# Kernel tuning notes

Hardware: AMD Instinct MI355X
Metric: run time of the kernel (lower is better)

Reference implementation:

```python
import jax, jax.numpy as jnp
import numpy as np

IN_DIM, HID, HEADS, LAYERS = 15, 128, 8, 6
N_NODES, N_EDGES = 20000, 160000
HC = HEADS * HID  # 1024
LN_EPS = 1e-5


def setup_inputs() -> dict:
    key = jax.random.key(0)
    ks = jax.random.split(key, 12)
    w = lambda k, shape: (jax.random.normal(k, shape, jnp.float32) * 0.02)
    return {
        "x": jax.random.normal(ks[0], (N_NODES, IN_DIM), jnp.float32),
        "edge_index": jax.random.randint(ks[1], (2, N_EDGES), 0, N_NODES, jnp.int32),
        # input projection
        "Win": w(ks[2], (IN_DIM, HID)), "b_in": jnp.zeros((HID,), jnp.float32),
        # per-layer TransformerConv params (stacked over LAYERS)
        "Wq": w(ks[3], (LAYERS, HID, HC)), "bq": jnp.zeros((LAYERS, HC), jnp.float32),
        "Wk": w(ks[4], (LAYERS, HID, HC)), "bk": jnp.zeros((LAYERS, HC), jnp.float32),
        "Wv": w(ks[5], (LAYERS, HID, HC)), "bv": jnp.zeros((LAYERS, HC), jnp.float32),
        "Wskip": w(ks[6], (LAYERS, HID, HC)), "bskip": jnp.zeros((LAYERS, HC), jnp.float32),
        "Wbeta": w(ks[7], (LAYERS, 3 * HC, 1)),  # lin_beta, bias=False
        # LayerNorm(hid*heads) and output proj per layer
        "ln_g": jnp.ones((LAYERS, HC), jnp.float32), "ln_b": jnp.zeros((LAYERS, HC), jnp.float32),
        "Wproj": w(ks[8], (LAYERS, HC, HID)), "bproj": jnp.zeros((LAYERS, HID), jnp.float32),
    }


def _transformer_layer(h, src, dst, Wq, bq, Wk, bk, Wv, bv, Wskip, bskip, Wbeta, ln_g, ln_b, Wproj, bproj):
    N = h.shape[0]
    # multi-head q/k/v: [N, H, C]
    q = (h @ Wq + bq).reshape(N, HEADS, HID)
    k = (h @ Wk + bk).reshape(N, HEADS, HID)
    v = (h @ Wv + bv).reshape(N, HEADS, HID)
    # per-edge attention logits: [E, H]
    alpha = jnp.einsum("ehc,ehc->eh", q[dst], k[src]) / jnp.sqrt(jnp.float32(HID))
    # segment softmax over incoming edges of each destination node
    amax = jax.ops.segment_max(alpha, dst, num_segments=N)  # [N, H]
    ex = jnp.exp(alpha - amax[dst])
    denom = jax.ops.segment_sum(ex, dst, num_segments=N)  # [N, H]
    attn = ex / (denom[dst] + 1e-16)  # [E, H]
    # weighted message scatter-sum: [N, H, C] -> concat [N, H*C]
    msg = v[src] * attn[:, :, None]
    out = jax.ops.segment_sum(msg, dst, num_segments=N).reshape(N, HC)
    # beta-gated skip (beta=True, concat=True)
    x_r = h @ Wskip + bskip  # [N, HC]
    beta = jax.nn.sigmoid(jnp.concatenate([out, x_r, out - x_r], axis=-1) @ Wbeta)  # [N, 1]
    out = beta * x_r + (1.0 - beta) * out
    # LayerNorm over last dim (HC)
    mu = jnp.mean(out, axis=-1, keepdims=True)
    var = jnp.var(out, axis=-1, keepdims=True)
    out = (out - mu) * jax.lax.rsqrt(var + LN_EPS) * ln_g + ln_b
    # project back, residual, relu
    out = out @ Wproj + bproj
    return jax.nn.relu(out + h)


def reference(x, edge_index, Win, b_in, Wq, bq, Wk, bk, Wv, bv, Wskip, bskip, Wbeta, ln_g, ln_b, Wproj, bproj):
    src, dst = edge_index[0], edge_index[1]
    h = x @ Win + b_in  # input_lin; dropout is identity in eval
    for l in range(LAYERS):
        h = _transformer_layer(h, src, dst, Wq[l], bq[l], Wk[l], bk[l], Wv[l], bv[l],
                               Wskip[l], bskip[l], Wbeta[l], ln_g[l], ln_b[l], Wproj[l], bproj[l])
    return h
```

## Files before the change

### kernel.cpp

```cpp
#include <hip/hip_runtime.h>
#include <stdint.h>

#define NN 20000
#define NE 160000
#define L_IN 15
#define D_H 128
#define N_HEADS 8
#define D_HC 1024
#define N_LAYERS 6
#define M_PAD 20096
#define QS2 2048

typedef unsigned short u16;
typedef __attribute__((ext_vector_type(8))) short short8;
typedef __attribute__((ext_vector_type(4))) float f32x4;

#define RSQRT_D 0.08838834764831845f

__device__ __forceinline__ float bu2f(u16 u) { return __uint_as_float(((unsigned)u) << 16); }
__device__ __forceinline__ u16 f2bu(float f) {
    unsigned x = __float_as_uint(f);
    return (u16)((x + 0x7fffu + ((x >> 16) & 1u)) >> 16);
}
__device__ __forceinline__ float wred64(float v) {
#pragma unroll
    for (int m = 32; m >= 1; m >>= 1) v += __shfl_xor(v, m, 64);
    return v;
}
__device__ __forceinline__ void cvt16(const uint4& u0, const uint4& u1, float* f) {
    unsigned d[8] = {u0.x, u0.y, u0.z, u0.w, u1.x, u1.y, u1.z, u1.w};
#pragma unroll
    for (int i = 0; i < 8; i++) {
        f[2 * i]     = __uint_as_float(d[i] << 16);
        f[2 * i + 1] = __uint_as_float(d[i] & 0xffff0000u);
    }
}

__global__ void k_detect(const u16* __restrict__ xb, int* __restrict__ flag) {
    int t = threadIdx.x;
    u16 u = xb[2 * t];
    int e = (u >> 7) & 0xFF;
    int weird = (e > 150 || (e != 0 && e < 100)) ? 1 : 0;
    __shared__ int cnt;
    if (t == 0) cnt = 0;
    __syncthreads();
    atomicAdd(&cnt, weird);
    __syncthreads();
    if (t == 0) *flag = (cnt > 64) ? 1 : 0;
}

struct CvDesc { const void* in[13]; u16* out[13]; };
#define CV_TOTAL 1930976
__global__ void k_convert_all(CvDesc dsc, const int* __restrict__ flag) {
    const int sizes[13] = {NN * L_IN, L_IN * D_H, D_H,
                           N_LAYERS * D_HC, N_LAYERS * D_HC, N_LAYERS * D_HC,
                           N_LAYERS * D_HC, N_LAYERS * 3 * D_HC,
                           N_LAYERS * D_HC, N_LAYERS * D_HC, N_LAYERS * D_H,
                           N_LAYERS * D_H * D_HC, N_LAYERS * D_H * D_HC};
    int off = blockIdx.x * 256 + threadIdx.x;
    if (off >= CV_TOTAL) return;
    int seg = 0;
#pragma unroll
    for (int s = 0; s < 13; s++) {
        if (off >= sizes[s] && seg == s) { off -= sizes[s]; seg = s + 1; }
    }
    if (*flag) dsc.out[seg][off] = f2bu(((const float*)dsc.in[seg])[off]);
    else       dsc.out[seg][off] = ((const u16*)dsc.in[seg])[off];
}

__global__ void k_zero(int* __restrict__ p, int n) {
    int i = blockIdx.x * 256 + threadIdx.x;
    if (i < n) p[i] = 0;
}

__global__ void k_convT_vs(const void* __restrict__ Wv, const void* __restrict__ Ws,
                           u16* __restrict__ WvT, u16* __restrict__ Bmain,
                           const int* __restrict__ flag) {
    __shared__ u16 tile[64][66];
    int tk = blockIdx.x, tn = blockIdx.y, l = blockIdx.z;
    int t = threadIdx.x;
    int isv = (tn < 16);
    const void* W = isv ? Wv : Ws;
    int n_off = (tn & 15) * 64;
    int r = t >> 2, c0 = (t & 3) * 16;
    size_t base = (size_t)l * 128 * 1024 + (size_t)(tk * 64 + r) * 1024 + n_off + c0;
    if (*flag) {
        const float* Wf = (const float*)W;
#pragma unroll
        for (int cc = 0; cc < 16; cc++) tile[c0 + cc][r] = f2bu(Wf[base + cc]);
    } else {
        const u16* Wh = (const u16*)W;
#pragma unroll
        for (int cc = 0; cc < 16; cc++) tile[c0 + cc][r] = Wh[base + cc];
    }
    __syncthreads();
    int i = t >> 2, j0 = (t & 3) * 16;
    u16* dst = isv ? (WvT + ((size_t)l * 1024 + n_off + i) * 128 + tk * 64 + j0)
                   : (Bmain + ((size_t)l * 2048 + 1024 + n_off + i) * 128 + tk * 64 + j0);
#pragma unroll
    for (int jj = 0; jj < 16; jj++) dst[jj] = tile[i][j0 + jj];
}

__global__ void k_convT_proj(const void* __restrict__ Wp, u16* __restrict__ WT,
                             const int* __restrict__ flag) {
    __shared__ u16 tile[64][66];
    int tk = blockIdx.x, tn = blockIdx.y, l = blockIdx.z;
    int t = threadIdx.x;
    int r = t >> 2, c0 = (t & 3) * 16;
    size_t base = (size_t)l * 1024 * 128 + (size_t)(tk * 64 + r) * 128 + tn * 64 + c0;
    if (*flag) {
        const float* Wf = (const float*)Wp;
#pragma unroll
        for (int cc = 0; cc < 16; cc++) tile[c0 + cc][r] = f2bu(Wf[base + cc]);
    } else {
        const u16* Wh = (const u16*)Wp;
#pragma unroll
        for (int cc = 0; cc < 16; cc++) tile[c0 + cc][r] = Wh[base + cc];
    }
    __syncthreads();
    int i = t >> 2, j0 = (t & 3) * 16;
    u16* dst = WT + ((size_t)l * 128 + tn * 64 + i) * 1024 + tk * 64 + j0;
#pragma unroll
    for (int jj = 0; jj < 16; jj++) dst[jj] = tile[i][j0 + jj];
}

__global__ void k_GG(const u16* __restrict__ Wqb, const u16* __restrict__ Wkb,
                     u16* __restrict__ Bmain) {
    int h = blockIdx.x, l = blockIdx.y;
    __shared__ __align__(16) u16 Als[128 * 32];
    __shared__ __align__(16) u16 Bls[128 * 32];
    const int t = threadIdx.x;
    const int wave = t >> 6, lane = t & 63, quad = lane >> 4, l16 = lane & 15;
    const int wm = (wave >> 1) * 64, wn = (wave & 1) * 64;
    const u16* Ab = Wqb + (size_t)l * 128 * 1024 + h * 128;
    const u16* Bb = Wkb + (size_t)l * 128 * 1024 + h * 128;
    f32x4 acc[4][4];
#pragma unroll
    for (int i = 0; i < 4; i++)
#pragma unroll
        for (int j = 0; j < 4; j++) acc[i][j] = (f32x4){0.f, 0.f, 0.f, 0.f};
    for (int ko = 0; ko < 128; ko += 32) {
#pragma unroll
        for (int c = t; c < 512; c += 256) {
            int row = c >> 2, kc = c & 3;
            *reinterpret_cast<uint4*>(&Als[row * 32 + kc * 8]) =
                *reinterpret_cast<const uint4*>(Ab + (size_t)row * 1024 + ko + kc * 8);
            *reinterpret_cast<uint4*>(&Bls[row * 32 + kc * 8]) =
                *reinterpret_cast<const uint4*>(Bb + (size_t)row * 1024 + ko + kc * 8);
        }
        __syncthreads();
        short8 af[4], bf[4];
#pragma unroll
        for (int mt = 0; mt < 4; mt++)
            af[mt] = *reinterpret_cast<const short8*>(&Als[(wm + mt * 16 + l16) * 32 + quad * 8]);
#pragma unroll
        for (int nt = 0; nt < 4; nt++)
            bf[nt] = *reinterpret_cast<const short8*>(&Bls[(wn + nt * 16 + l16) * 32 + quad * 8]);
#pragma unroll
        for (int mt = 0; mt < 4; mt++)
#pragma unroll
            for (int nt = 0; nt < 4; nt++)
                acc[mt][nt] = __builtin_amdgcn_mfma_f32_16x16x32_bf16(af[mt], bf[nt], acc[mt][nt], 0, 0, 0);
        __syncthreads();
    }
    u16* dst = Bmain + (size_t)l * 2048 * 128;
#pragma unroll
    for (int mt = 0; mt < 4; mt++)
#pragma unroll
        for (int r = 0; r < 4; r++) {
            int row = wm + mt * 16 + quad * 4 + r;
#pragma unroll
            for (int nt = 0; nt < 4; nt++) {
                int col = wn + nt * 16 + l16;
                dst[(size_t)(h * 128 + col) * 128 + row] = f2bu(acc[mt][nt][r] * RSQRT_D);
            }
        }
}

__global__ void k_pre_small(const u16* __restrict__ Wqb, const u16* __restrict__ Wkb,
                            const u16* __restrict__ bq, const u16* __restrict__ bk,
                            u16* __restrict__ cb, float* __restrict__ wscT,
                            float* __restrict__ csc) {
    int gid = blockIdx.x * 256 + threadIdx.x;
    if (gid >= N_LAYERS * 2056) return;
    int l = gid / 2056, r = gid % 2056;
    float acc = 0.f;
    if (r < 1024) {
        int h = r >> 7, b = r & 127;
        const u16* bqp = bq + l * D_HC + h * 128;
        const u16* wkp = Wkb + (size_t)l * 128 * 1024 + (size_t)b * 1024 + h * 128;
        for (int m = 0; m < 128; m++) acc += bu2f(bqp[m]) * bu2f(wkp[m]);
        cb[l * 1024 + r] = f2bu(acc * RSQRT_D);
    } else if (r < 2048) {
        int idx = r - 1024;
        int h = idx >> 7, a = idx & 127;
        const u16* wqp = Wqb + (size_t)l * 128 * 1024 + (size_t)a * 1024 + h * 128;
        const u16* bkp = bk + l * D_HC + h * 128;
        for (int m = 0; m < 128; m++) acc += bu2f(wqp[m]) * bu2f(bkp[m]);
        wscT[l * 1024 + idx] = acc * RSQRT_D;
    } else {
        int h = r - 2048;
        const u16* bqp = bq + l * D_HC + h * 128;
        const u16* bkp = bk + l * D_HC + h * 128;
        for (int m = 0; m < 128; m++) acc += bu2f(bqp[m]) * bu2f(bkp[m]);
        csc[l * 8 + h] = acc * RSQRT_D;
    }
}

__global__ void k_input_proj(const u16* __restrict__ x, const u16* __restrict__ Win,
                             const u16* __restrict__ b_in, u16* __restrict__ h) {
    int gid = blockIdx.x * 256 + threadIdx.x;
    int n = gid >> 7, j = gid & 127;
    float acc = bu2f(b_in[j]);
#pragma unroll
    for (int i = 0; i < L_IN; i++) acc += bu2f(x[n * L_IN + i]) * bu2f(Win[i * D_H + j]);
    h[gid] = f2bu(acc);
}

__global__ void k_hist(const int* __restrict__ dst, int* __restrict__ cnt) {
    int e = blockIdx.x * 256 + threadIdx.x;
    if (e < NE) atomicAdd(&cnt[dst[e]], 1);
}
__global__ void k_scanA(const int* __restrict__ cnt, int* __restrict__ incl, int* __restrict__ bsum) {
    __shared__ int s[256];
    int b = blockIdx.x, t = threadIdx.x, i = b * 256 + t;
    int v = (i < NN) ? cnt[i] : 0;
    s[t] = v;
    __syncthreads();
    for (int off = 1; off < 256; off <<= 1) {
        int u = (t >= off) ? s[t - off] : 0;
        __syncthreads();
        s[t] += u;
        __syncthreads();
    }
    if (i < NN) incl[i] = s[t];
    if (t == 255) bsum[b] = s[255];
}
__global__ void k_scanB(const int* __restrict__ bsum, int* __restrict__ bpre, int nb) {
    __shared__ int s[128];
    int t = threadIdx.x;
    int v = (t < nb) ? bsum[t] : 0;
    s[t] = v;
    __syncthreads();
    for (int off = 1; off < 128; off <<= 1) {
        int u = (t >= off) ? s[t - off] : 0;
        __syncthreads();
        s[t] += u;
        __syncthreads();
    }
    if (t < nb) bpre[t] = s[t] - v;
}
__global__ void k_scanC(const int* __restrict__ incl, const int* __restrict__ bpre, int* __restrict__ offs) {
    int b = blockIdx.x, t = threadIdx.x, i = b * 256 + t;
    if (i < NN) offs[i + 1] = incl[i] + bpre[b];
    if (i == 0) offs[0] = 0;
}
__global__ void k_scatter(const int* __restrict__ dst, const int* __restrict__ src,
                          const int* __restrict__ offs, int* __restrict__ cursor,
                          int* __restrict__ srcp) {
    int e = blockIdx.x * 256 + threadIdx.x;
    if (e < NE) {
        int d = dst[e];
        int p = offs[d] + atomicAdd(&cursor[d], 1);
        srcp[p] = src[e];
    }
}

__global__ void k_gemm(const u16* __restrict__ A, int lda, int K,
                       const u16* __restrict__ Bt,
                       u16* __restrict__ C, int ldc,
                       const u16* __restrict__ bia0, const u16* __restrict__ bia1) {
    __shared__ __align__(16) u16 smem[128 * 136];
    u16* Als = smem;
    u16* Bls = smem + 4096;
    const int m0 = blockIdx.y * 128, n0 = blockIdx.x * 128;
    const int t = threadIdx.x;
    const int wave = t >> 6, lane = t & 63, quad = lane >> 4, l16 = lane & 15;
    const int wm = (wave >> 1) * 64, wn = (wave & 1) * 64;
    f32x4 acc[4][4];
#pragma unroll
    for (int i = 0; i < 4; i++)
#pragma unroll
        for (int j = 0; j < 4; j++) acc[i][j] = (f32x4){0.f, 0.f, 0.f, 0.f};

    for (int ko = 0; ko < K; ko += 32) {
#pragma unroll
        for (int c = t; c < 512; c += 256) {
            int row = c >> 2, kc = c & 3;
            *reinterpret_cast<uint4*>(&Als[row * 32 + kc * 8]) =
                *reinterpret_cast<const uint4*>(A + (size_t)(m0 + row) * lda + ko + kc * 8);
            *reinterpret_cast<uint4*>(&Bls[row * 32 + kc * 8]) =
                *reinterpret_cast<const uint4*>(Bt + (size_t)(n0 + row) * K + ko + kc * 8);
        }
        __syncthreads();
        short8 af[4], bf[4];
#pragma unroll
        for (int mt = 0; mt < 4; mt++)
            af[mt] = *reinterpret_cast<const short8*>(&Als[(wm + mt * 16 + l16) * 32 + quad * 8]);
#pragma unroll
        for (int nt = 0; nt < 4; nt++)
            bf[nt] = *reinterpret_cast<const short8*>(&Bls[(wn + nt * 16 + l16) * 32 + quad * 8]);
#pragma unroll
        for (int mt = 0; mt < 4; mt++)
#pragma unroll
            for (int nt = 0; nt < 4; nt++)
                acc[mt][nt] = __builtin_amdgcn_mfma_f32_16x16x32_bf16(af[mt], bf[nt], acc[mt][nt], 0, 0, 0);
        __syncthreads();
    }
#pragma unroll
    for (int mt = 0; mt < 4; mt++)
#pragma unroll
        for (int r = 0; r < 4; r++) {
            int rl = wm + mt * 16 + quad * 4 + r;
#pragma unroll
            for (int nt = 0; nt < 4; nt++) {
                int cl = wn + nt * 16 + l16;
                int col = n0 + cl;
                const u16* bp = (col < 1024) ? bia0 : bia1;
                smem[rl * 136 + cl] = f2bu(acc[mt][nt][r] + bu2f(bp[col & 1023]));
            }
        }
    __syncthreads();
#pragma unroll
    for (int c = t; c < 2048; c += 256) {
        int row = c >> 4, kc = c & 15;
        int grow = m0 + row;
        if (grow < NN)
            *reinterpret_cast<uint4*>(C + (size_t)grow * ldc + n0 + kc * 8) =
                *reinterpret_cast<const uint4*>(&smem[row * 136 + kc * 8]);
    }
}

__global__ void k_attn2(u16* __restrict__ qkvs2, const u16* __restrict__ hc,
                        const int* __restrict__ offs, const int* __restrict__ srcp,
                        const float* __restrict__ wscT_l, const float* __restrict__ csc_l) {
    int gid = blockIdx.x * 256 + threadIdx.x;
    int d = gid >> 6, lane = gid & 63;
    if (d >= NN) return;
    int hh = lane >> 3, ci = (lane & 7) * 16;
    u16* zp = qkvs2 + (size_t)d * QS2 + hh * 128 + ci;
    float zf[16];
    {
        uint4 z0 = *reinterpret_cast<const uint4*>(zp);
        uint4 z1 = *reinterpret_cast<const uint4*>(zp + 8);
        cvt16(z0, z1, zf);
    }
    float scown;
    {
        const u16* hdp = hc + (size_t)d * 128 + ci;
        uint4 hd0 = *reinterpret_cast<const uint4*>(hdp);
        uint4 hd1 = *reinterpret_cast<const uint4*>(hdp + 8);
        float hdf[16];
        cvt16(hd0, hd1, hdf);
        const float* wt = wscT_l + hh * 128 + ci;
        float scp = 0.f;
#pragma unroll
        for (int j = 0; j < 16; j++) scp += hdf[j] * wt[j];
        scp += __shfl_xor(scp, 1, 64);
        scp += __shfl_xor(scp, 2, 64);
        scp += __shfl_xor(scp, 4, 64);
        scown = scp + csc_l[hh];
    }
    float u[16];
#pragma unroll
    for (int j = 0; j < 16; j++) u[j] = 0.f;
    float lrun = 0.f;

    int beg = offs[d], end = offs[d + 1];
    for (int c0 = beg; c0 < end; c0 += 64) {
        int cn = min(64, end - c0);
        int myidx = (c0 + lane < end) ? srcp[c0 + lane] : 0;
        int s = __shfl(myidx, 0, 64);
        const u16* hp = hc + (size_t)s * 128 + ci;
        uint4 a0 = *reinterpret_cast<const uint4*>(hp);
        uint4 a1 = *reinterpret_cast<const uint4*>(hp + 8);
        for (int i = 0; i < cn; i++) {
            uint4 n0 = a0, n1 = a1;
            if (i + 1 < cn) {
                int sn = __shfl(myidx, i + 1, 64);
                const u16* hpn = hc + (size_t)sn * 128 + ci;
                n0 = *reinterpret_cast<const uint4*>(hpn);
                n1 = *reinterpret_cast<const uint4*>(hpn + 8);
            }
            float hf[16];
            cvt16(a0, a1, hf);
            float p = 0.f;
#pragma unroll
            for (int j = 0; j < 16; j++) p += zf[j] * hf[j];
            p += __shfl_xor(p, 1, 64);
            p += __shfl_xor(p, 2, 64);
            p += __shfl_xor(p, 4, 64);
            float w = __expf(p + scown);
            lrun += w;
#pragma unroll
            for (int j = 0; j < 16; j++) u[j] += w * hf[j];
            a0 = n0; a1 = n1;
        }
    }
    float inv = 1.f / (lrun + 1e-16f);
    unsigned out[8];
#pragma unroll
    for (int j = 0; j < 8; j++)
        out[j] = (unsigned)f2bu(u[2 * j] * inv) | ((unsigned)f2bu(u[2 * j + 1] * inv) << 16);
    uint4* op = reinterpret_cast<uint4*>(zp);
    op[0] = make_uint4(out[0], out[1], out[2], out[3]);
    op[1] = make_uint4(out[4], out[5], out[6], out[7]);
}

__global__ void k_vproj(const u16* __restrict__ A ,
                        const u16* __restrict__ WvT_l, const u16* __restrict__ bv_l,
                        u16* __restrict__ obuf) {
    __shared__ __align__(16) u16 smem[128 * 136];
    u16* Als = smem;
    u16* Bls = smem + 4096;
    const int m0 = blockIdx.x * 128, h = blockIdx.y;
    const int t = threadIdx.x;
    const int wave = t >> 6, lane = t & 63, quad = lane >> 4, l16 = lane & 15;
    const int wm = (wave >> 1) * 64, wn = (wave & 1) * 64;
    f32x4 acc[4][4];
#pragma unroll
    for (int i = 0; i < 4; i++)
#pragma unroll
        for (int j = 0; j < 4; j++) acc[i][j] = (f32x4){0.f, 0.f, 0.f, 0.f};

    for (int ko = 0; ko < 128; ko += 32) {
#pragma unroll
        for (int c = t; c < 512; c += 256) {
            int row = c >> 2, kc = c & 3;
            *reinterpret_cast<uint4*>(&Als[row * 32 + kc * 8]) =
                *reinterpret_cast<const uint4*>(A + (size_t)(m0 + row) * QS2 + h * 128 + ko + kc * 8);
            *reinterpret_cast<uint4*>(&Bls[row * 32 + kc * 8]) =
                *reinterpret_cast<const uint4*>(WvT_l + (size_t)(h * 128 + row) * 128 + ko + kc * 8);
        }
        __syncthreads();
        short8 af[4], bf[4];
#pragma unroll
        for (int mt = 0; mt < 4; mt++)
            af[mt] = *reinterpret_cast<const short8*>(&Als[(wm + mt * 16 + l16) * 32 + quad * 8]);
#pragma unroll
        for (int nt = 0; nt < 4; nt++)
            bf[nt] = *reinterpret_cast<const short8*>(&Bls[(wn + nt * 16 + l16) * 32 + quad * 8]);
#pragma unroll
        for (int mt = 0; mt < 4; mt++)
#pragma unroll
            for (int nt = 0; nt < 4; nt++)
                acc[mt][nt] = __builtin_amdgcn_mfma_f32_16x16x32_bf16(af[mt], bf[nt], acc[mt][nt], 0, 0, 0);
        __syncthreads();
    }
#pragma unroll
    for (int mt = 0; mt < 4; mt++)
#pragma unroll
        for (int r = 0; r < 4; r++) {
            int rl = wm + mt * 16 + quad * 4 + r;
#pragma unroll
            for (int nt = 0; nt < 4; nt++) {
                int cl = wn + nt * 16 + l16;
                smem[rl * 136 + cl] = f2bu(acc[mt][nt][r] + bu2f(bv_l[h * 128 + cl]));
            }
        }
    __syncthreads();
#pragma unroll
    for (int c = t; c < 2048; c += 256) {
        int row = c >> 4, kc = c & 15;
        int grow = m0 + row;
        if (grow < NN)
            *reinterpret_cast<uint4*>(obuf + (size_t)grow * 1024 + h * 128 + kc * 8) =
                *reinterpret_cast<const uint4*>(&smem[row * 136 + kc * 8]);
    }
}

__global__ void k_betaLN(const u16* __restrict__ obuf, u16* __restrict__ qkvs2,
                         const u16* __restrict__ Wb, const u16* __restrict__ lng,
                         const u16* __restrict__ lnb) {
    int gid = blockIdx.x * 256 + threadIdx.x;
    int d = gid >> 6, lane = gid & 63;
    if (d >= NN) return;
    int c0 = lane * 16;
    float o[16], xr[16];
    {
        const u16* op = obuf + (size_t)d * 1024 + c0;
        uint4 o0 = *reinterpret_cast<const uint4*>(op);
        uint4 o1 = *reinterpret_cast<const uint4*>(op + 8);
        cvt16(o0, o1, o);
        const u16* xp = qkvs2 + (size_t)d * QS2 + 1024 + c0;
        uint4 x0 = *reinterpret_cast<const uint4*>(xp);
        uint4 x1 = *reinterpret_cast<const uint4*>(xp + 8);
        cvt16(x0, x1, xr);
    }
    float part = 0.f;
    {
        const u16* wp = Wb + c0;
        uint4 u0 = *reinterpret_cast<const uint4*>(wp);
        uint4 u1 = *reinterpret_cast<const uint4*>(wp + 8);
        float wf[16];
        cvt16(u0, u1, wf);
#pragma unroll
        for (int j = 0; j < 16; j++) part += o[j] * wf[j];
        u0 = *reinterpret_cast<const uint4*>(wp + D_HC);
        u1 = *reinterpret_cast<const uint4*>(wp + D_HC + 8);
        cvt16(u0, u1, wf);
#pragma unroll
        for (int j = 0; j < 16; j++) part += xr[j] * wf[j];
        u0 = *reinterpret_cast<const uint4*>(wp + 2 * D_HC);
        u1 = *reinterpret_cast<const uint4*>(wp + 2 * D_HC + 8);
        cvt16(u0, u1, wf);
#pragma unroll
        for (int j = 0; j < 16; j++) part += (o[j] - xr[j]) * wf[j];
    }
    float logit = wred64(part);
    float beta = 1.f / (1.f + __expf(-logit));
    float g[16], s1 = 0.f, s2 = 0.f;
#pragma unroll
    for (int j = 0; j < 16; j++) {
        g[j] = beta * xr[j] + (1.f - beta) * o[j];
        s1 += g[j]; s2 += g[j] * g[j];
    }
    s1 = wred64(s1);
    s2 = wred64(s2);
    float mu = s1 * (1.f / 1024.f);
    float var = s2 * (1.f / 1024.f) - mu * mu;
    float rs = rsqrtf(var + 1e-5f);
    {
        const u16* gp = lng + c0;
        const u16* bp2 = lnb + c0;
        uint4 g0 = *reinterpret_cast<const uint4*>(gp);
        uint4 g1 = *reinterpret_cast<const uint4*>(gp + 8);
        uint4 b0 = *reinterpret_cast<const uint4*>(bp2);
        uint4 b1 = *reinterpret_cast<const uint4*>(bp2 + 8);
        float lgf[16], lbf[16];
        cvt16(g0, g1, lgf);
        cvt16(b0, b1, lbf);
        unsigned out[8];
#pragma unroll
        for (int j = 0; j < 8; j++) {
            float y0 = (g[2 * j] - mu) * rs * lgf[2 * j] + lbf[2 * j];
            float y1 = (g[2 * j + 1] - mu) * rs * lgf[2 * j + 1] + lbf[2 * j + 1];
            out[j] = (unsigned)f2bu(y0) | ((unsigned)f2bu(y1) << 16);
        }
        uint4* yp = reinterpret_cast<uint4*>(qkvs2 + (size_t)d * QS2 + c0);
        yp[0] = make_uint4(out[0], out[1], out[2], out[3]);
        yp[1] = make_uint4(out[4], out[5], out[6], out[7]);
    }
}

#define PLDA 40
__global__ void k_proj(const u16* __restrict__ A, int lda,
                       const u16* __restrict__ Bt,
                       void* __restrict__ C, int mode,
                       const u16* __restrict__ bias, const u16* __restrict__ resid,
                       const int* __restrict__ flag) {
    __shared__ __align__(16) u16 Als[32 * PLDA];
    __shared__ __align__(16) u16 Bls[128 * PLDA];
    const int m0 = blockIdx.x * 32;
    const int t = threadIdx.x;
    const int wave = t >> 6, lane = t & 63, quad = lane >> 4, l16 = lane & 15;
    const int fp32out = (mode == 2 && *flag) ? 1 : 0;
    f32x4 acc[2][2];
#pragma unroll
    for (int i = 0; i < 2; i++)
#pragma unroll
        for (int j = 0; j < 2; j++) acc[i][j] = (f32x4){0.f, 0.f, 0.f, 0.f};

    uint4 pa, pb0, pb1;
    const int arow = t >> 2, akc = t & 3;
    const int b0row = t >> 2, b0kc = t & 3;
    const int b1row = (t + 256) >> 2, b1kc = t & 3;
    {
        if (t < 128)
            pa = *reinterpret_cast<const uint4*>(A + (size_t)(m0 + arow) * lda + akc * 8);
        pb0 = *reinterpret_cast<const uint4*>(Bt + (size_t)b0row * 1024 + b0kc * 8);
        pb1 = *reinterpret_cast<const uint4*>(Bt + (size_t)b1row * 1024 + b1kc * 8);
    }
    for (int ko = 0; ko < 1024; ko += 32) {
        if (t < 128)
            *reinterpret_cast<uint4*>(&Als[arow * PLDA + akc * 8]) = pa;
        *reinterpret_cast<uint4*>(&Bls[b0row * PLDA + b0kc * 8]) = pb0;
        *reinterpret_cast<uint4*>(&Bls[b1row * PLDA + b1kc * 8]) = pb1;
        __syncthreads();
        int kn = ko + 32;
        if (kn < 1024) {
            if (t < 128)
                pa = *reinterpret_cast<const uint4*>(A + (size_t)(m0 + arow) * lda + kn + akc * 8);
            pb0 = *reinterpret_cast<const uint4*>(Bt + (size_t)b0row * 1024 + kn + b0kc * 8);
            pb1 = *reinterpret_cast<const uint4*>(Bt + (size_t)b1row * 1024 + kn + b1kc * 8);
        }
        short8 af[2], bf[2];
#pragma unroll
        for (int mt = 0; mt < 2; mt++)
            af[mt] = *reinterpret_cast<const short8*>(&Als[(mt * 16 + l16) * PLDA + quad * 8]);
#pragma unroll
        for (int nt = 0; nt < 2; nt++)
            bf[nt] = *reinterpret_cast<const short8*>(&Bls[(wave * 32 + nt * 16 + l16) * PLDA + quad * 8]);
#pragma unroll
        for (int mt = 0; mt < 2; mt++)
#pragma unroll
            for (int nt = 0; nt < 2; nt++)
                acc[mt][nt] = __builtin_amdgcn_mfma_f32_16x16x32_bf16(af[mt], bf[nt], acc[mt][nt], 0, 0, 0);
        __syncthreads();
    }
#pragma unroll
    for (int mt = 0; mt < 2; mt++)
#pragma unroll
    for (int r = 0; r < 4; r++) {
        int row = m0 + mt * 16 + quad * 4 + r;
        if (row >= NN) continue;
#pragma unroll
        for (int nt = 0; nt < 2; nt++) {
            int col = wave * 32 + nt * 16 + l16;
            float v = acc[mt][nt][r] + bu2f(bias[col]) + bu2f(resid[(size_t)row * D_H + col]);
            float rr = (v == v) ? fmaxf(v, 0.f) : v;
            if (fp32out) ((float*)C)[(size_t)row * D_H + col] = rr;
            else         ((u16*)C)[(size_t)row * D_H + col] = f2bu(rr);
        }
    }
}

extern "C" void kernel_launch(void* const* d_in, const int* in_sizes, int n_in,
                              void* d_out, int out_size, void* d_ws, size_t ws_size,
                              hipStream_t stream) {
    const int* ei = (const int*)d_in[1];
    const int* srcI = ei;
    const int* dstI = ei + NE;

    char* w = (char*)d_ws;
    auto carve = [&](size_t bytes) -> char* {
        char* p = w;
        w += (bytes + 255) & ~(size_t)255;
        return p;
    };
    u16* Bmain  = (u16*)carve((size_t)N_LAYERS * 2048 * 128 * 2);
    u16* WvT    = (u16*)carve((size_t)N_LAYERS * 1024 * 128 * 2);
    u16* WTp    = (u16*)carve((size_t)N_LAYERS * 128 * 1024 * 2);
    u16* hA     = (u16*)carve((size_t)M_PAD * D_H * 2);
    u16* hB     = (u16*)carve((size_t)M_PAD * D_H * 2);
    u16* qkvs2  = (u16*)carve((size_t)M_PAD * QS2 * 2);
    u16* obuf   = (u16*)carve((size_t)M_PAD * 1024 * 2);
    u16* cbuf   = (u16*)carve((size_t)N_LAYERS * 1024 * 2);
    float* wscb = (float*)carve((size_t)N_LAYERS * 1024 * 4);
    float* cscb = (float*)carve((size_t)N_LAYERS * 8 * 4);
    int* cnt    = (int*)carve(2 * NN * 4);
    int* cursor = cnt + NN;
    int* offs   = (int*)carve((NN + 1) * 4);
    int* incl   = (int*)carve(NN * 4);
    int* bsum   = (int*)carve(128 * 4);
    int* bpre   = (int*)carve(128 * 4);
    int* srcp   = (int*)carve(NE * 4);
    int* flag   = (int*)carve(256);

    const int conv_size[13] = {NN * L_IN, L_IN * D_H, D_H,
                               N_LAYERS * D_HC, N_LAYERS * D_HC, N_LAYERS * D_HC,
                               N_LAYERS * D_HC, N_LAYERS * 3 * D_HC,
                               N_LAYERS * D_HC, N_LAYERS * D_HC, N_LAYERS * D_H,
                               N_LAYERS * D_H * D_HC, N_LAYERS * D_H * D_HC};
    const int conv_idx[13] = {0, 2, 3, 5, 7, 9, 11, 12, 13, 14, 16, 4, 6};
    CvDesc dsc;
    u16* conv[13];
    for (int i = 0; i < 13; i++) {
        conv[i] = (u16*)carve((size_t)conv_size[i] * 2);
        dsc.in[i] = d_in[conv_idx[i]];
        dsc.out[i] = conv[i];
    }

    k_detect<<<1, 256, 0, stream>>>((const u16*)d_in[0], flag);
    k_convert_all<<<(CV_TOTAL + 255) / 256, 256, 0, stream>>>(dsc, flag);
    const u16* x    = conv[0];
    const u16* Win  = conv[1];
    const u16* b_in = conv[2];
    const u16* bq   = conv[3];
    const u16* bk   = conv[4];
    const u16* bv   = conv[5];
    const u16* bsk  = conv[6];
    const u16* Wb   = conv[7];
    const u16* lng  = conv[8];
    const u16* lnb  = conv[9];
    const u16* bp   = conv[10];
    const u16* Wqb  = conv[11];
    const u16* Wkb  = conv[12];

    k_convT_vs<<<dim3(2, 32, 6), 256, 0, stream>>>(d_in[8], d_in[10], WvT, Bmain, flag);
    k_convT_proj<<<dim3(16, 2, 6), 256, 0, stream>>>(d_in[15], WTp, flag);
    k_GG<<<dim3(8, 6), 256, 0, stream>>>(Wqb, Wkb, Bmain);
    k_pre_small<<<(N_LAYERS * 2056 + 255) / 256, 256, 0, stream>>>(Wqb, Wkb, bq, bk,
                                                                   cbuf, wscb, cscb);
    k_input_proj<<<(NN * D_H) / 256, 256, 0, stream>>>(x, Win, b_in, hA);
    k_zero<<<(2 * NN + 255) / 256, 256, 0, stream>>>(cnt, 2 * NN);
    k_hist<<<(NE + 255) / 256, 256, 0, stream>>>(dstI, cnt);
    const int NB = (NN + 255) / 256;
    k_scanA<<<NB, 256, 0, stream>>>(cnt, incl, bsum);
    k_scanB<<<1, 128, 0, stream>>>(bsum, bpre, NB);
    k_scanC<<<NB, 256, 0, stream>>>(incl, bpre, offs);
    k_scatter<<<(NE + 255) / 256, 256, 0, stream>>>(dstI, srcI, offs, cursor, srcp);

    u16* hc = hA;
    u16* hn = hB;
    for (int l = 0; l < N_LAYERS; l++) {
        k_gemm<<<dim3(16, 157), 256, 0, stream>>>(hc, D_H, D_H,
                                                  Bmain + (size_t)l * 2048 * 128,
                                                  qkvs2, QS2,
                                                  cbuf + l * 1024, bsk + l * D_HC);
        k_attn2<<<(NN * 64) / 256, 256, 0, stream>>>(qkvs2, hc, offs, srcp,
                                                     wscb + l * 1024, cscb + l * 8);
        k_vproj<<<dim3(157, 8), 256, 0, stream>>>(qkvs2, WvT + (size_t)l * 1024 * 128,
                                                  bv + l * D_HC, obuf);
        k_betaLN<<<(NN * 64) / 256, 256, 0, stream>>>(obuf, qkvs2,
                                                      Wb + (size_t)l * 3 * D_HC,
                                                      lng + l * D_HC, lnb + l * D_HC);
        int last = (l == N_LAYERS - 1);
        void* outp = last ? d_out : (void*)hn;
        k_proj<<<628, 256, 0, stream>>>(qkvs2, QS2, WTp + (size_t)l * 128 * 1024,
                                        outp, last ? 2 : 1,
                                        bp + l * D_H, hc, flag);
        u16* tmp = hc; hc = hn; hn = tmp;
    }
}
```

Baseline: 907.6 us.

## Fuse beta-gate LayerNorm into output projection GEMM via shared memory

Merges the beta/LayerNorm kernel and the output projection kernel into one kernel. Each block normalizes 16 rows into shared memory and then runs the MFMA projection directly from LDS. This drops a kernel launch and the global write and re-read of the normalized activations. In exchange, tiles shrink to 16 rows, so the weight matrix is re-read by twice as many blocks, and LDS use per block goes up.

```diff
diff --git a/kernel.cpp b/kernel.cpp
--- a/kernel.cpp
+++ b/kernel.cpp
@@ -469,148 +469,124 @@
     }
 }
 
-__global__ void k_betaLN(const u16* __restrict__ obuf, u16* __restrict__ qkvs2,
-                         const u16* __restrict__ Wb, const u16* __restrict__ lng,
-                         const u16* __restrict__ lnb) {
-    int gid = blockIdx.x * 256 + threadIdx.x;
-    int d = gid >> 6, lane = gid & 63;
-    if (d >= NN) return;
-    int c0 = lane * 16;
-    float o[16], xr[16];
-    {
-        const u16* op = obuf + (size_t)d * 1024 + c0;
-        uint4 o0 = *reinterpret_cast<const uint4*>(op);
-        uint4 o1 = *reinterpret_cast<const uint4*>(op + 8);
-        cvt16(o0, o1, o);
-        const u16* xp = qkvs2 + (size_t)d * QS2 + 1024 + c0;
-        uint4 x0 = *reinterpret_cast<const uint4*>(xp);
-        uint4 x1 = *reinterpret_cast<const uint4*>(xp + 8);
-        cvt16(x0, x1, xr);
-    }
-    float part = 0.f;
-    {
-        const u16* wp = Wb + c0;
-        uint4 u0 = *reinterpret_cast<const uint4*>(wp);
-        uint4 u1 = *reinterpret_cast<const uint4*>(wp + 8);
-        float wf[16];
-        cvt16(u0, u1, wf);
-#pragma unroll
-        for (int j = 0; j < 16; j++) part += o[j] * wf[j];
-        u0 = *reinterpret_cast<const uint4*>(wp + D_HC);
-        u1 = *reinterpret_cast<const uint4*>(wp + D_HC + 8);
-        cvt16(u0, u1, wf);
-#pragma unroll
-        for (int j = 0; j < 16; j++) part += xr[j] * wf[j];
-        u0 = *reinterpret_cast<const uint4*>(wp + 2 * D_HC);
-        u1 = *reinterpret_cast<const uint4*>(wp + 2 * D_HC + 8);
-        cvt16(u0, u1, wf);
-#pragma unroll
-        for (int j = 0; j < 16; j++) part += (o[j] - xr[j]) * wf[j];
-    }
-    float logit = wred64(part);
-    float beta = 1.f / (1.f + __expf(-logit));
-    float g[16], s1 = 0.f, s2 = 0.f;
-#pragma unroll
-    for (int j = 0; j < 16; j++) {
-        g[j] = beta * xr[j] + (1.f - beta) * o[j];
-        s1 += g[j]; s2 += g[j] * g[j];
-    }
-    s1 = wred64(s1);
-    s2 = wred64(s2);
-    float mu = s1 * (1.f / 1024.f);
-    float var = s2 * (1.f / 1024.f) - mu * mu;
-    float rs = rsqrtf(var + 1e-5f);
-    {
-        const u16* gp = lng + c0;
-        const u16* bp2 = lnb + c0;
-        uint4 g0 = *reinterpret_cast<const uint4*>(gp);
-        uint4 g1 = *reinterpret_cast<const uint4*>(gp + 8);
-        uint4 b0 = *reinterpret_cast<const uint4*>(bp2);
-        uint4 b1 = *reinterpret_cast<const uint4*>(bp2 + 8);
-        float lgf[16], lbf[16];
-        cvt16(g0, g1, lgf);
-        cvt16(b0, b1, lbf);
-        unsigned out[8];
-#pragma unroll
-        for (int j = 0; j < 8; j++) {
-            float y0 = (g[2 * j] - mu) * rs * lgf[2 * j] + lbf[2 * j];
-            float y1 = (g[2 * j + 1] - mu) * rs * lgf[2 * j + 1] + lbf[2 * j + 1];
-            out[j] = (unsigned)f2bu(y0) | ((unsigned)f2bu(y1) << 16);
-        }
-        uint4* yp = reinterpret_cast<uint4*>(qkvs2 + (size_t)d * QS2 + c0);
-        yp[0] = make_uint4(out[0], out[1], out[2], out[3]);
-        yp[1] = make_uint4(out[4], out[5], out[6], out[7]);
-    }
-}
-
 #define PLDA 40
-__global__ void k_proj(const u16* __restrict__ A, int lda,
-                       const u16* __restrict__ Bt,
-                       void* __restrict__ C, int mode,
-                       const u16* __restrict__ bias, const u16* __restrict__ resid,
-                       const int* __restrict__ flag) {
-    __shared__ __align__(16) u16 Als[32 * PLDA];
+#define YLD 1032
+__global__ void k_bproj(const u16* __restrict__ obuf, const u16* __restrict__ qkvs2,
+                        const u16* __restrict__ Wb, const u16* __restrict__ lng,
+                        const u16* __restrict__ lnb,
+                        const u16* __restrict__ Bt ,
+                        void* __restrict__ C, int mode,
+                        const u16* __restrict__ bias, const u16* __restrict__ resid,
+                        const int* __restrict__ flag) {
+    __shared__ __align__(16) u16 yls[16 * YLD];
     __shared__ __align__(16) u16 Bls[128 * PLDA];
-    const int m0 = blockIdx.x * 32;
+    const int m0 = blockIdx.x * 16;
     const int t = threadIdx.x;
     const int wave = t >> 6, lane = t & 63, quad = lane >> 4, l16 = lane & 15;
     const int fp32out = (mode == 2 && *flag) ? 1 : 0;
-    f32x4 acc[2][2];
-#pragma unroll
-    for (int i = 0; i < 2; i++)
-#pragma unroll
-        for (int j = 0; j < 2; j++) acc[i][j] = (f32x4){0.f, 0.f, 0.f, 0.f};
-
-    uint4 pa, pb0, pb1;
-    const int arow = t >> 2, akc = t & 3;
-    const int b0row = t >> 2, b0kc = t & 3;
-    const int b1row = (t + 256) >> 2, b1kc = t & 3;
+
+    uint4 pb0, pb1;
+    const int b0row = t >> 2, bkc = t & 3;
+    const int b1row = (t + 256) >> 2;
+    pb0 = *reinterpret_cast<const uint4*>(Bt + (size_t)b0row * 1024 + bkc * 8);
+    pb1 = *reinterpret_cast<const uint4*>(Bt + (size_t)b1row * 1024 + bkc * 8);
+
     {
-        if (t < 128)
-            pa = *reinterpret_cast<const uint4*>(A + (size_t)(m0 + arow) * lda + akc * 8);
-        pb0 = *reinterpret_cast<const uint4*>(Bt + (size_t)b0row * 1024 + b0kc * 8);
-        pb1 = *reinterpret_cast<const uint4*>(Bt + (size_t)b1row * 1024 + b1kc * 8);
-    }
+        int c0 = lane * 16;
+        float wf1[16], wf2[16], wf3[16], lgf[16], lbf[16];
+        {
+            const u16* wp = Wb + c0;
+            uint4 u0 = *reinterpret_cast<const uint4*>(wp);
+            uint4 u1 = *reinterpret_cast<const uint4*>(wp + 8);
+            cvt16(u0, u1, wf1);
+            u0 = *reinterpret_cast<const uint4*>(wp + D_HC);
+            u1 = *reinterpret_cast<const uint4*>(wp + D_HC + 8);
+            cvt16(u0, u1, wf2);
+            u0 = *reinterpret_cast<const uint4*>(wp + 2 * D_HC);
+            u1 = *reinterpret_cast<const uint4*>(wp + 2 * D_HC + 8);
+            cvt16(u0, u1, wf3);
+            u0 = *reinterpret_cast<const uint4*>(lng + c0);
+            u1 = *reinterpret_cast<const uint4*>(lng + c0 + 8);
+            cvt16(u0, u1, lgf);
+            u0 = *reinterpret_cast<const uint4*>(lnb + c0);
+            u1 = *reinterpret_cast<const uint4*>(lnb + c0 + 8);
+            cvt16(u0, u1, lbf);
+        }
+        for (int rr = 0; rr < 4; rr++) {
+            int row = wave * 4 + rr;
+            int d = m0 + row;
+            float o[16], xr[16];
+            {
+                const u16* op = obuf + (size_t)d * 1024 + c0;
+                uint4 o0 = *reinterpret_cast<const uint4*>(op);
+                uint4 o1 = *reinterpret_cast<const uint4*>(op + 8);
+                cvt16(o0, o1, o);
+                const u16* xp = qkvs2 + (size_t)d * QS2 + 1024 + c0;
+                uint4 x0 = *reinterpret_cast<const uint4*>(xp);
+                uint4 x1 = *reinterpret_cast<const uint4*>(xp + 8);
+                cvt16(x0, x1, xr);
+            }
+            float part = 0.f;
+#pragma unroll
+            for (int j = 0; j < 16; j++)
+                part += o[j] * wf1[j] + xr[j] * wf2[j] + (o[j] - xr[j]) * wf3[j];
+            float logit = wred64(part);
+            float beta = 1.f / (1.f + __expf(-logit));
+            float g[16], s1 = 0.f, s2 = 0.f;
+#pragma unroll
+            for (int j = 0; j < 16; j++) {
+                g[j] = beta * xr[j] + (1.f - beta) * o[j];
+                s1 += g[j]; s2 += g[j] * g[j];
+            }
+            s1 = wred64(s1);
+            s2 = wred64(s2);
+            float mu = s1 * (1.f / 1024.f);
+            float var = s2 * (1.f / 1024.f) - mu * mu;
+            float rs = rsqrtf(var + 1e-5f);
+            unsigned yo[8];
+#pragma unroll
+            for (int j = 0; j < 8; j++) {
+                float y0 = (g[2 * j] - mu) * rs * lgf[2 * j] + lbf[2 * j];
+                float y1 = (g[2 * j + 1] - mu) * rs * lgf[2 * j + 1] + lbf[2 * j + 1];
+                yo[j] = (unsigned)f2bu(y0) | ((unsigned)f2bu(y1) << 16);
+            }
+            uint4* yp = reinterpret_cast<uint4*>(&yls[row * YLD + c0]);
+            yp[0] = make_uint4(yo[0], yo[1], yo[2], yo[3]);
+            yp[1] = make_uint4(yo[4], yo[5], yo[6], yo[7]);
+        }
+    }
+    __syncthreads();
+
+    f32x4 acc[2];
+    acc[0] = (f32x4){0.f, 0.f, 0.f, 0.f};
+    acc[1] = (f32x4){0.f, 0.f, 0.f, 0.f};
     for (int ko = 0; ko < 1024; ko += 32) {
-        if (t < 128)
-            *reinterpret_cast<uint4*>(&Als[arow * PLDA + akc * 8]) = pa;
-        *reinterpret_cast<uint4*>(&Bls[b0row * PLDA + b0kc * 8]) = pb0;
-        *reinterpret_cast<uint4*>(&Bls[b1row * PLDA + b1kc * 8]) = pb1;
+        *reinterpret_cast<uint4*>(&Bls[b0row * PLDA + bkc * 8]) = pb0;
+        *reinterpret_cast<uint4*>(&Bls[b1row * PLDA + bkc * 8]) = pb1;
         __syncthreads();
         int kn = ko + 32;
         if (kn < 1024) {
-            if (t < 128)
-                pa = *reinterpret_cast<const uint4*>(A + (size_t)(m0 + arow) * lda + kn + akc * 8);
-            pb0 = *reinterpret_cast<const uint4*>(Bt + (size_t)b0row * 1024 + kn + b0kc * 8);
-            pb1 = *reinterpret_cast<const uint4*>(Bt + (size_t)b1row * 1024 + kn + b1kc * 8);
-        }
-        short8 af[2], bf[2];
-#pragma unroll
-        for (int mt = 0; mt < 2; mt++)
-            af[mt] = *reinterpret_cast<const short8*>(&Als[(mt * 16 + l16) * PLDA + quad * 8]);
-#pragma unroll
-        for (int nt = 0; nt < 2; nt++)
-            bf[nt] = *reinterpret_cast<const short8*>(&Bls[(wave * 32 + nt * 16 + l16) * PLDA + quad * 8]);
-#pragma unroll
-        for (int mt = 0; mt < 2; mt++)
-#pragma unroll
-            for (int nt = 0; nt < 2; nt++)
-                acc[mt][nt] = __builtin_amdgcn_mfma_f32_16x16x32_bf16(af[mt], bf[nt], acc[mt][nt], 0, 0, 0);
-        __syncthreads();
-    }
-#pragma unroll
-    for (int mt = 0; mt < 2; mt++)
+            pb0 = *reinterpret_cast<const uint4*>(Bt + (size_t)b0row * 1024 + kn + bkc * 8);
+            pb1 = *reinterpret_cast<const uint4*>(Bt + (size_t)b1row * 1024 + kn + bkc * 8);
+        }
+        short8 af = *reinterpret_cast<const short8*>(&yls[l16 * YLD + ko + quad * 8]);
+#pragma unroll
+        for (int nt = 0; nt < 2; nt++) {
+            short8 bf = *reinterpret_cast<const short8*>(&Bls[(wave * 32 + nt * 16 + l16) * PLDA + quad * 8]);
+            acc[nt] = __builtin_amdgcn_mfma_f32_16x16x32_bf16(af, bf, acc[nt], 0, 0, 0);
+        }
+        __syncthreads();
+    }
 #pragma unroll
     for (int r = 0; r < 4; r++) {
-        int row = m0 + mt * 16 + quad * 4 + r;
-        if (row >= NN) continue;
+        int row = m0 + quad * 4 + r;
 #pragma unroll
         for (int nt = 0; nt < 2; nt++) {
             int col = wave * 32 + nt * 16 + l16;
-            float v = acc[mt][nt][r] + bu2f(bias[col]) + bu2f(resid[(size_t)row * D_H + col]);
-            float rr = (v == v) ? fmaxf(v, 0.f) : v;
-            if (fp32out) ((float*)C)[(size_t)row * D_H + col] = rr;
-            else         ((u16*)C)[(size_t)row * D_H + col] = f2bu(rr);
+            float v = acc[nt][r] + bu2f(bias[col]) + bu2f(resid[(size_t)row * D_H + col]);
+            float rr2 = (v == v) ? fmaxf(v, 0.f) : v;
+            if (fp32out) ((float*)C)[(size_t)row * D_H + col] = rr2;
+            else         ((u16*)C)[(size_t)row * D_H + col] = f2bu(rr2);
         }
     }
 }
@@ -702,14 +678,14 @@
                                                      wscb + l * 1024, cscb + l * 8);
         k_vproj<<<dim3(157, 8), 256, 0, stream>>>(qkvs2, WvT + (size_t)l * 1024 * 128,
                                                   bv + l * D_HC, obuf);
-        k_betaLN<<<(NN * 64) / 256, 256, 0, stream>>>(obuf, qkvs2,
-                                                      Wb + (size_t)l * 3 * D_HC,
-                                                      lng + l * D_HC, lnb + l * D_HC);
         int last = (l == N_LAYERS - 1);
         void* outp = last ? d_out : (void*)hn;
-        k_proj<<<628, 256, 0, stream>>>(qkvs2, QS2, WTp + (size_t)l * 128 * 1024,
-                                        outp, last ? 2 : 1,
-                                        bp + l * D_H, hc, flag);
+        k_bproj<<<NN / 16, 256, 0, stream>>>(obuf, qkvs2,
+                                             Wb + (size_t)l * 3 * D_HC,
+                                             lng + l * D_HC, lnb + l * D_HC,
+                                             WTp + (size_t)l * 128 * 1024,
+                                             outp, last ? 2 : 1,
+                                             bp + l * D_H, hc, flag);
         u16* tmp = hc; hc = hn; hn = tmp;
     }
 }
```

New measurement: 991.3 us. 9.2% more time.
